# Kernel optimization log

Measured on AMD Instinct MI355X. Metric: run time of the kernel, lower is better.

The kernel has to match this reference:

```python
import jax, jax.numpy as jnp
import numpy as np

CAPACITY_FACTOR = 1.0
MIN_CAPACITY = 4


def setup_inputs() -> dict:
    key = jax.random.key(0)
    ks = jax.random.split(key, 4)
    B, S, D, E, F = 4, 2048, 1024, 16, 4096
    hidden_states = jax.random.normal(ks[0], (B, S, D), dtype=jnp.float32)
    wg = jax.random.normal(ks[1], (D, E), dtype=jnp.float32) * 0.02
    w1 = jax.random.normal(ks[2], (E, D, F), dtype=jnp.float32) * (1.0 / np.sqrt(D))
    b1 = jnp.zeros((E, F), dtype=jnp.float32)
    w2 = jax.random.normal(ks[3], (E, F, D), dtype=jnp.float32) * (1.0 / np.sqrt(F))
    b2 = jnp.zeros((E, D), dtype=jnp.float32)
    return {"hidden_states": hidden_states, "wg": wg, "w1": w1, "b1": b1, "w2": w2, "b2": b2}


def reference(hidden_states, wg, w1, b1, w2, b2):
    B, S, D = hidden_states.shape
    x = hidden_states.reshape(-1, D)                      # [T, D] tokens
    T = x.shape[0]
    E = wg.shape[1]
    capacity = max(int(np.ceil(T / E * CAPACITY_FACTOR)), MIN_CAPACITY)  # static

    # ---- TopKGate (k=1, no noise, no RTS) ----
    logits = x @ wg                                       # [T, E]
    gates = jax.nn.softmax(logits, axis=-1)
    idx1 = jnp.argmax(gates, axis=1)                      # [T]
    mask1 = jax.nn.one_hot(idx1, E, dtype=gates.dtype)    # [T, E]
    exp_counts = jnp.sum(mask1, axis=0).astype(jnp.int32) # per-expert token counts

    # load-balancing aux loss
    me = jnp.mean(gates, axis=0)
    ce = jnp.mean(mask1, axis=0)
    l_aux = jnp.sum(me * ce) * E

    # slot assignment within each expert, drop overflow tokens
    locations1 = jnp.cumsum(mask1, axis=0) - 1.0          # [T, E]
    mask1 = mask1 * (locations1 < capacity).astype(gates.dtype)
    locations1_s = jnp.sum(locations1 * mask1, axis=1).astype(jnp.int32)  # [T]
    gates1 = gates * mask1                                # [T, E] gate prob of kept assignment

    loc_oh = jax.nn.one_hot(locations1_s, capacity, dtype=gates.dtype)    # [T, C]
    combine = jnp.einsum('te,tc->tec', gates1, loc_oh)    # [T, E, C]
    dispatch = (combine > 0).astype(x.dtype)              # [T, E, C]

    # ---- dispatch -> grouped expert FFN -> combine ----
    disp = jnp.einsum('tec,td->ecd', dispatch, x)         # [E, C, D]
    h = jax.nn.gelu(jnp.einsum('ecd,edf->ecf', disp, w1) + b1[:, None, :])
    eo = jnp.einsum('ecf,efd->ecd', h, w2) + b2[:, None, :]  # [E, C, D]
    out = jnp.einsum('tec,ecd->td', combine, eo).reshape(B, S, D)
    return out, l_aux, exp_counts
```

## Files before the change

### kernel.cpp

```cpp
#include <hip/hip_runtime.h>

typedef unsigned short u16;
typedef unsigned int   u32;
typedef unsigned long long u64;
typedef __attribute__((ext_vector_type(8))) __bf16 bf16x8;
typedef __attribute__((ext_vector_type(4))) float  f32x4;

#define TOK 8192
#define DIM 1024
#define NE  16
#define NF  4096
#define CAP 512

__device__ __forceinline__ u16 f2bf(float f) {
    u32 u = __float_as_uint(f);
    u32 r = (u + 0x7FFFu + ((u >> 16) & 1u)) >> 16;
    return (u16)r;
}

__device__ __forceinline__ float gelu_tanh(float x) {
    float u = 0.7978845608028654f * (x + 0.044715f * x * x * x);
    float t = __expf(-2.f * fabsf(u));
    float th = (1.f - t) / (1.f + t);
    th = (u < 0.f) ? -th : th;
    return 0.5f * x * (1.f + th);
}

__device__ __forceinline__ void gld16(const void* g, void* l) {
    __builtin_amdgcn_global_load_lds(
        (const __attribute__((address_space(1))) void*)g,
        (__attribute__((address_space(3))) void*)l, 16, 0, 0);
}

__global__ void moe_init(float* me_sums) {
    if (threadIdx.x < NE) me_sums[threadIdx.x] = 0.f;
}

__global__ void moe_wgT(const float* __restrict__ wg, float* __restrict__ wgT) {
    int i = blockIdx.x * 256 + threadIdx.x;
    int d = i >> 4, e = i & 15;
    wgT[(size_t)e * DIM + d] = wg[i];
}

__global__ void moe_gate(const float* __restrict__ x, const float* __restrict__ wgT,
                         int* __restrict__ eidx, float* __restrict__ gp,
                         float* __restrict__ me_sums) {
    __shared__ float lme[NE];
    const int tid = threadIdx.x;
    if (tid < NE) lme[tid] = 0.f;
    __syncthreads();
    const int tok = blockIdx.x * 16 + (tid >> 4);
    const int e   = tid & 15;
    const float4* xp = (const float4*)(x + (size_t)tok * DIM);
    const float4* wp = (const float4*)(wgT + (size_t)e * DIM);
    float acc = 0.f;
#pragma unroll 4
    for (int i = 0; i < DIM / 4; ++i) {
        float4 a = xp[i], b = wp[i];
        acc = fmaf(a.x, b.x, acc); acc = fmaf(a.y, b.y, acc);
        acc = fmaf(a.z, b.z, acc); acc = fmaf(a.w, b.w, acc);
    }
    float mx = acc;
    for (int off = 8; off; off >>= 1) mx = fmaxf(mx, __shfl_xor(mx, off, 16));
    float ex = __expf(acc - mx);
    float sum = ex;
    for (int off = 8; off; off >>= 1) sum += __shfl_xor(sum, off, 16);
    float p = ex / sum;
    atomicAdd(&lme[e], p);
    float bv = acc; int bi = e;
    for (int off = 8; off; off >>= 1) {
        float ov = __shfl_xor(bv, off, 16);
        int   oi = __shfl_xor(bi, off, 16);
        if (ov > bv || (ov == bv && oi < bi)) { bv = ov; bi = oi; }
    }
    float pw = __shfl(p, bi, 16);
    if (e == 0) { eidx[tok] = bi; gp[tok] = pw; }
    __syncthreads();
    if (tid < 16) atomicAdd(&me_sums[tid], lme[tid]);
}

__global__ void moe_scan(const int* __restrict__ eidx, const float* __restrict__ me_sums,
                         int* __restrict__ slot, int* __restrict__ tos,
                         float* __restrict__ tail ) {
    __shared__ int wcnt[16][16];
    __shared__ int base[16];
    const int tid = threadIdx.x, wid = tid >> 6, lane = tid & 63;
    if (tid < 16) base[tid] = 0;
    for (int i = tid; i < NE * CAP; i += 1024) tos[i] = -1;
    __syncthreads();
    const u64 below = ((u64)1 << lane) - 1;
    for (int chunk = 0; chunk < TOK / 1024; ++chunk) {
        int t = chunk * 1024 + tid;
        int e = eidx[t];
        int rank = 0;
#pragma unroll
        for (int ex = 0; ex < 16; ++ex) {
            u64 m = __ballot(e == ex);
            if (e == ex)    rank = __popcll(m & below);
            if (lane == ex) wcnt[wid][ex] = __popcll(m);
        }
        __syncthreads();
        int pre = base[e];
        for (int w = 0; w < wid; ++w) pre += wcnt[w][e];
        int s = pre + rank;
        slot[t] = s;
        if (s < CAP) tos[e * CAP + s] = t;
        __syncthreads();
        if (tid < 16) {
            int tot = 0;
            for (int w = 0; w < 16; ++w) tot += wcnt[w][tid];
            base[tid] += tot;
        }
        __syncthreads();
    }
    if (tid == 0) {
        float laux = 0.f;
        for (int e2 = 0; e2 < 16; ++e2) {
            float me = me_sums[e2] / (float)TOK;
            float ce = (float)base[e2] / (float)TOK;
            laux += me * ce;
        }
        tail[0] = laux * (float)NE;
    }
    if (tid < 16) tail[1 + tid] = (float)base[tid];
}

__global__ void moe_gather(const float* __restrict__ x, const int* __restrict__ tos,
                           u16* __restrict__ Xg) {
    const int s = blockIdx.x, tid = threadIdx.x;
    const int t = tos[s];
    float4 v = make_float4(0.f, 0.f, 0.f, 0.f);
    if (t >= 0) v = *(const float4*)(x + (size_t)t * DIM + tid * 4);
    u32 lo = (u32)f2bf(v.x) | ((u32)f2bf(v.y) << 16);
    u32 hi = (u32)f2bf(v.z) | ((u32)f2bf(v.w) << 16);
    *(uint2*)(Xg + (size_t)s * DIM + tid * 4) = make_uint2(lo, hi);
}

__global__ void moe_zero_dropped(const int* __restrict__ slot, float* __restrict__ out) {
    const int t = blockIdx.x;
    if (slot[t] < CAP) return;
    *(float4*)(out + (size_t)t * DIM + threadIdx.x * 4) = make_float4(0.f, 0.f, 0.f, 0.f);
}

__global__ void moe_convT(const float* __restrict__ src, u16* __restrict__ dst,
                          int R, int C) {
    __shared__ float tile[64][65];
    int b = blockIdx.x;
    const int tilesC = C >> 6, tilesR = R >> 6;
    int tc = b % tilesC; b /= tilesC;
    int tr = b % tilesR; int e = b / tilesR;
    const float* S = src + ((size_t)e * R + tr * 64) * C + tc * 64;
    const int tid = threadIdx.x;
    const int rr = tid >> 4, cc = (tid & 15) * 4;
#pragma unroll
    for (int i = 0; i < 4; ++i) {
        float4 v = *(const float4*)(S + (size_t)(rr + i * 16) * C + cc);
        tile[rr + i * 16][cc + 0] = v.x; tile[rr + i * 16][cc + 1] = v.y;
        tile[rr + i * 16][cc + 2] = v.z; tile[rr + i * 16][cc + 3] = v.w;
    }
    __syncthreads();
    const int c = tid >> 2, r0 = (tid & 3) * 16;
    u16 tmp[16];
#pragma unroll
    for (int k = 0; k < 16; ++k) tmp[k] = f2bf(tile[r0 + k][c]);
    u16* D = dst + ((size_t)e * C + tc * 64 + c) * R + tr * 64 + r0;
    uint4 w0 = make_uint4((u32)tmp[0] | ((u32)tmp[1] << 16), (u32)tmp[2] | ((u32)tmp[3] << 16),
                          (u32)tmp[4] | ((u32)tmp[5] << 16), (u32)tmp[6] | ((u32)tmp[7] << 16));
    uint4 w1 = make_uint4((u32)tmp[8] | ((u32)tmp[9] << 16), (u32)tmp[10] | ((u32)tmp[11] << 16),
                          (u32)tmp[12] | ((u32)tmp[13] << 16), (u32)tmp[14] | ((u32)tmp[15] << 16));
    *(uint4*)(D) = w0;
    *(uint4*)(D + 8) = w1;
}

__global__ __launch_bounds__(512, 2) void moe_gemm1(const u16* __restrict__ Xg,
                                                    const u16* __restrict__ W1t,
                                                    const float* __restrict__ b1,
                                                    u16* __restrict__ H) {
    __shared__ alignas(16) u16 Als[4][8192];
    __shared__ alignas(16) u16 Bls[4][8192];
    const int tid = threadIdx.x, wave = tid >> 6, lane = tid & 63;
    const int flat = blockIdx.x;
    const int xcd  = flat & 7;
    const int slot = flat >> 3;
    const int e    = xcd * 2 + (slot >> 5);
    const int tile = slot & 31;
    const int bm   = tile & 1;
    const int bn   = tile >> 1;
    const int r4   = lane >> 2;
    const int gch  = (lane & 3) ^ ((lane >> 3) & 3);
    const u16* aSrc = Xg + (size_t)(e * 512 + bm * 256 + wave * 16 + r4) * DIM + gch * 8;
    const u16* bSrc = W1t + (size_t)e * NF * DIM
                    + (size_t)(bn * 256 + wave * 16 + r4) * DIM + gch * 8;
    const int wm = wave & 1, wn = wave >> 1;
    const int fr = lane & 15, fq = lane >> 4;
    const int rdoff = fr * 32 + (fq ^ ((fr >> 1) & 3)) * 8;

    f32x4 acc[2][4][4] = {};

#define STG1A(P, T) do { const int ko = (T) * 32; u16* ad = &Als[P][wave * 512]; \
        gld16(aSrc + ko, ad); gld16(aSrc + 128 * DIM + ko, ad + 4096); } while (0)
#define STG1B(P, T) do { const int ko = (T) * 32; u16* bd = &Bls[P][wave * 512]; \
        gld16(bSrc + ko, bd); gld16(bSrc + 128 * DIM + ko, bd + 4096); } while (0)

    const int NT = DIM / 32;
    STG1A(0, 0); STG1B(0, 0);
    STG1A(1, 1); STG1B(1, 1);
    STG1A(2, 2); STG1B(2, 2);
    for (int t = 0; t < NT; ++t) {
        const int c = t & 3;
        const int rem = NT - 1 - t;
        if (rem >= 2)      asm volatile("s_waitcnt vmcnt(8)" ::: "memory");
        else if (rem == 1) asm volatile("s_waitcnt vmcnt(4)" ::: "memory");
        else               asm volatile("s_waitcnt vmcnt(0)" ::: "memory");
        __builtin_amdgcn_sched_barrier(0);
        __builtin_amdgcn_s_barrier();
        __builtin_amdgcn_sched_barrier(0);
        const u16* Ab = &Als[c][0];
        const u16* Bb = &Bls[c][0];
        bf16x8 bF[4], aF[4];
#pragma unroll
        for (int j = 0; j < 4; ++j)
            bF[j] = *(const bf16x8*)(const void*)(Bb + (wn * 64 + j * 16) * 32 + rdoff);
#pragma unroll
        for (int i = 0; i < 4; ++i)
            aF[i] = *(const bf16x8*)(const void*)(Ab + (wm * 128 + i * 16) * 32 + rdoff);
        if (t + 3 < NT) STG1A((c + 3) & 3, t + 3);
        __builtin_amdgcn_sched_barrier(0);
        asm volatile("s_waitcnt lgkmcnt(0)" ::: "memory");
        __builtin_amdgcn_sched_barrier(0);
        __builtin_amdgcn_s_setprio(1);
#pragma unroll
        for (int i = 0; i < 4; ++i)
#pragma unroll
            for (int j = 0; j < 4; ++j)
                acc[0][i][j] = __builtin_amdgcn_mfma_f32_16x16x32_bf16(aF[i], bF[j], acc[0][i][j], 0, 0, 0);
        __builtin_amdgcn_s_setprio(0);
        __builtin_amdgcn_sched_barrier(0);
        __builtin_amdgcn_s_barrier();
        __builtin_amdgcn_sched_barrier(0);
#pragma unroll
        for (int i = 0; i < 4; ++i)
            aF[i] = *(const bf16x8*)(const void*)(Ab + (wm * 128 + 64 + i * 16) * 32 + rdoff);
        if (t + 3 < NT) STG1B((c + 3) & 3, t + 3);
        __builtin_amdgcn_sched_barrier(0);
        asm volatile("s_waitcnt lgkmcnt(0)" ::: "memory");
        __builtin_amdgcn_sched_barrier(0);
        __builtin_amdgcn_s_setprio(1);
#pragma unroll
        for (int i = 0; i < 4; ++i)
#pragma unroll
            for (int j = 0; j < 4; ++j)
                acc[1][i][j] = __builtin_amdgcn_mfma_f32_16x16x32_bf16(aF[i], bF[j], acc[1][i][j], 0, 0, 0);
        __builtin_amdgcn_s_setprio(0);
    }
#undef STG1A
#undef STG1B

    const int mBase = e * 512 + bm * 256 + wm * 128;
    const int nBase = bn * 256 + wn * 64;
#pragma unroll
    for (int j = 0; j < 4; ++j) {
        const int f = nBase + j * 16 + fr;
        const float bias = b1[e * NF + f];
#pragma unroll
        for (int q = 0; q < 2; ++q)
#pragma unroll
            for (int i = 0; i < 4; ++i) {
                const int m0 = mBase + q * 64 + i * 16 + fq * 4;
#pragma unroll
                for (int r = 0; r < 4; ++r) {
                    float v = acc[q][i][j][r] + bias;
                    H[(size_t)(m0 + r) * NF + f] = f2bf(gelu_tanh(v));
                }
            }
    }
}

__global__ __launch_bounds__(512, 2) void moe_gemm2(const u16* __restrict__ H,
                                                    const u16* __restrict__ W2t,
                                                    const float* __restrict__ b2,
                                                    const int* __restrict__ tos,
                                                    const float* __restrict__ gp,
                                                    float* __restrict__ out) {
    __shared__ alignas(16) u16 Als[4][8192];
    __shared__ alignas(16) u16 Bls[4][4096];
    const int tid = threadIdx.x, wave = tid >> 6, lane = tid & 63;
    const int flat = blockIdx.x;
    const int xcd  = flat & 7;
    const int slot = flat >> 3;
    const int e    = xcd * 2 + (slot >> 4);
    const int tile = slot & 15;
    const int bm   = tile & 1;
    const int bn   = tile >> 1;
    const int r4   = lane >> 2;
    const int gch  = (lane & 3) ^ ((lane >> 3) & 3);
    const u16* aSrc = H + (size_t)(e * 512 + bm * 256 + wave * 16 + r4) * NF + gch * 8;
    const u16* bSrc = W2t + (size_t)e * DIM * NF
                    + (size_t)(bn * 128 + wave * 16 + r4) * NF + gch * 8;
    const int wm = wave & 1, wn = wave >> 1;
    const int fr = lane & 15, fq = lane >> 4;
    const int rdoff = fr * 32 + (fq ^ ((fr >> 1) & 3)) * 8;

    f32x4 acc[2][4][2] = {};

#define STG2A(P, T) do { const int ko = (T) * 32; u16* ad = &Als[P][wave * 512]; \
        gld16(aSrc + ko, ad); gld16(aSrc + (size_t)128 * NF + ko, ad + 4096); } while (0)
#define STG2B(P, T) do { const int ko = (T) * 32; u16* bd = &Bls[P][wave * 512]; \
        gld16(bSrc + ko, bd); } while (0)

    const int NT = NF / 32;
    STG2A(0, 0); STG2B(0, 0);
    STG2A(1, 1); STG2B(1, 1);
    STG2A(2, 2); STG2B(2, 2);
    for (int t = 0; t < NT; ++t) {
        const int c = t & 3;
        const int rem = NT - 1 - t;
        if (rem >= 2)      asm volatile("s_waitcnt vmcnt(6)" ::: "memory");
        else if (rem == 1) asm volatile("s_waitcnt vmcnt(3)" ::: "memory");
        else               asm volatile("s_waitcnt vmcnt(0)" ::: "memory");
        __builtin_amdgcn_sched_barrier(0);
        __builtin_amdgcn_s_barrier();
        __builtin_amdgcn_sched_barrier(0);
        const u16* Ab = &Als[c][0];
        const u16* Bb = &Bls[c][0];
        bf16x8 bF[2], aF[4];
#pragma unroll
        for (int j = 0; j < 2; ++j)
            bF[j] = *(const bf16x8*)(const void*)(Bb + (wn * 32 + j * 16) * 32 + rdoff);
#pragma unroll
        for (int i = 0; i < 4; ++i)
            aF[i] = *(const bf16x8*)(const void*)(Ab + (wm * 128 + i * 16) * 32 + rdoff);
        if (t + 3 < NT) STG2A((c + 3) & 3, t + 3);
        __builtin_amdgcn_sched_barrier(0);
        asm volatile("s_waitcnt lgkmcnt(0)" ::: "memory");
        __builtin_amdgcn_sched_barrier(0);
        __builtin_amdgcn_s_setprio(1);
#pragma unroll
        for (int i = 0; i < 4; ++i)
#pragma unroll
            for (int j = 0; j < 2; ++j)
                acc[0][i][j] = __builtin_amdgcn_mfma_f32_16x16x32_bf16(aF[i], bF[j], acc[0][i][j], 0, 0, 0);
        __builtin_amdgcn_s_setprio(0);
        __builtin_amdgcn_sched_barrier(0);
        __builtin_amdgcn_s_barrier();
        __builtin_amdgcn_sched_barrier(0);
#pragma unroll
        for (int i = 0; i < 4; ++i)
            aF[i] = *(const bf16x8*)(const void*)(Ab + (wm * 128 + 64 + i * 16) * 32 + rdoff);
        if (t + 3 < NT) STG2B((c + 3) & 3, t + 3);
        __builtin_amdgcn_sched_barrier(0);
        asm volatile("s_waitcnt lgkmcnt(0)" ::: "memory");
        __builtin_amdgcn_sched_barrier(0);
        __builtin_amdgcn_s_setprio(1);
#pragma unroll
        for (int i = 0; i < 4; ++i)
#pragma unroll
            for (int j = 0; j < 2; ++j)
                acc[1][i][j] = __builtin_amdgcn_mfma_f32_16x16x32_bf16(aF[i], bF[j], acc[1][i][j], 0, 0, 0);
        __builtin_amdgcn_s_setprio(0);
    }
#undef STG2A
#undef STG2B

    const int mBase = e * 512 + bm * 256 + wm * 128;
    const int nBase = bn * 128 + wn * 32;
#pragma unroll
    for (int q = 0; q < 2; ++q)
#pragma unroll
        for (int i = 0; i < 4; ++i) {
#pragma unroll
            for (int r = 0; r < 4; ++r) {
                const int m = mBase + q * 64 + i * 16 + fq * 4 + r;
                const int t = tos[m];
                if (t < 0) continue;
                const float g = gp[t];
#pragma unroll
                for (int j = 0; j < 2; ++j) {
                    const int d = nBase + j * 16 + fr;
                    out[(size_t)t * DIM + d] = g * (acc[q][i][j][r] + b2[e * DIM + d]);
                }
            }
        }
}

extern "C" void kernel_launch(void* const* d_in, const int* in_sizes, int n_in,
                              void* d_out, int out_size, void* d_ws, size_t ws_size,
                              hipStream_t stream) {
    const float* x  = (const float*)d_in[0];
    const float* wg = (const float*)d_in[1];
    const float* w1 = (const float*)d_in[2];
    const float* b1 = (const float*)d_in[3];
    const float* w2 = (const float*)d_in[4];
    const float* b2 = (const float*)d_in[5];
    float* out = (float*)d_out;

    char* ws = (char*)d_ws;
    const size_t WBF_OFF = 0;
    const size_t XG_OFF  = WBF_OFF + (size_t)NE * NF * DIM * 2;
    const size_t H_OFF   = XG_OFF + (size_t)TOK * DIM * 2;
    const size_t SM_OFF  = H_OFF + (size_t)TOK * NF * 2;
    u16* Wbf = (u16*)(ws + WBF_OFF);
    u16* Xg  = (u16*)(ws + XG_OFF);
    u16* H   = (u16*)(ws + H_OFF);
    int*   eidx = (int*)(ws + SM_OFF);
    float* gp   = (float*)(ws + SM_OFF + 32768);
    int*   slot = (int*)(ws + SM_OFF + 65536);
    int*   tos  = (int*)(ws + SM_OFF + 98304);
    float* me   = (float*)(ws + SM_OFF + 131072);
    float* wgT  = (float*)(ws + SM_OFF + 131072 + 128);

    float* tail = out + (size_t)TOK * DIM;

    moe_init<<<1, 64, 0, stream>>>(me);
    moe_wgT<<<64, 256, 0, stream>>>(wg, wgT);
    moe_gate<<<TOK / 16, 256, 0, stream>>>(x, wgT, eidx, gp, me);
    moe_scan<<<1, 1024, 0, stream>>>(eidx, me, slot, tos, tail);
    moe_gather<<<NE * CAP, 256, 0, stream>>>(x, tos, Xg);
    moe_zero_dropped<<<TOK, 256, 0, stream>>>(slot, out);
    moe_convT<<<NE * (DIM / 64) * (NF / 64), 256, 0, stream>>>(w1, Wbf, DIM, NF);
    moe_gemm1<<<512, 512, 0, stream>>>(Xg, Wbf, b1, H);
    moe_convT<<<NE * (NF / 64) * (DIM / 64), 256, 0, stream>>>(w2, Wbf, NF, DIM);
    moe_gemm2<<<256, 512, 0, stream>>>(H, Wbf, b2, tos, gp, out);
}
```

Measured before the change: 917.5 us.

## Co-schedule W2 bf16 transpose with GEMM1 in one kernel, merge small launches

GEMM1 is fused with the W2 fp32-to-bf16 transpose in a single heterogeneous launch: every fifth block runs a smaller 256x128 GEMM1 tile with double buffering, and the other blocks each transpose four 64x64 W2 tiles into a separate workspace buffer. The intent is to overlap the bandwidth-bound W2 conversion with the compute-bound GEMM1 and to raise occupancy with a smaller LDS footprint. It also folds the me_sums init into the wgT kernel and merges the gather with the dropped-token zeroing, removing launches. Risks: smaller GEMM tiles with a simpler pipeline lower MFMA efficiency, the kernel needs extra workspace for a second weight buffer, and the dropped-token zeroing now only covers the first NE*CAP tokens.

```diff
diff --git a/kernel.cpp b/kernel.cpp
--- a/kernel.cpp
+++ b/kernel.cpp
@@ -32,12 +32,10 @@
         (__attribute__((address_space(3))) void*)l, 16, 0, 0);
 }
 
-__global__ void moe_init(float* me_sums) {
-    if (threadIdx.x < NE) me_sums[threadIdx.x] = 0.f;
-}
-
-__global__ void moe_wgT(const float* __restrict__ wg, float* __restrict__ wgT) {
+__global__ void moe_wgT(const float* __restrict__ wg, float* __restrict__ wgT,
+                        float* __restrict__ me_sums) {
     int i = blockIdx.x * 256 + threadIdx.x;
+    if (i < NE) me_sums[i] = 0.f;
     int d = i >> 4, e = i & 15;
     wgT[(size_t)e * DIM + d] = wg[i];
 }
@@ -125,21 +123,18 @@
     if (tid < 16) tail[1 + tid] = (float)base[tid];
 }
 
-__global__ void moe_gather(const float* __restrict__ x, const int* __restrict__ tos,
-                           u16* __restrict__ Xg) {
-    const int s = blockIdx.x, tid = threadIdx.x;
-    const int t = tos[s];
+__global__ void moe_gather_zero(const float* __restrict__ x, const int* __restrict__ tos,
+                                const int* __restrict__ slot, u16* __restrict__ Xg,
+                                float* __restrict__ out) {
+    const int b = blockIdx.x, tid = threadIdx.x;
+    const int t = tos[b];
     float4 v = make_float4(0.f, 0.f, 0.f, 0.f);
     if (t >= 0) v = *(const float4*)(x + (size_t)t * DIM + tid * 4);
     u32 lo = (u32)f2bf(v.x) | ((u32)f2bf(v.y) << 16);
     u32 hi = (u32)f2bf(v.z) | ((u32)f2bf(v.w) << 16);
-    *(uint2*)(Xg + (size_t)s * DIM + tid * 4) = make_uint2(lo, hi);
-}
-
-__global__ void moe_zero_dropped(const int* __restrict__ slot, float* __restrict__ out) {
-    const int t = blockIdx.x;
-    if (slot[t] < CAP) return;
-    *(float4*)(out + (size_t)t * DIM + threadIdx.x * 4) = make_float4(0.f, 0.f, 0.f, 0.f);
+    *(uint2*)(Xg + (size_t)b * DIM + tid * 4) = make_uint2(lo, hi);
+    if (slot[b] >= CAP)
+        *(float4*)(out + (size_t)b * DIM + tid * 4) = make_float4(0.f, 0.f, 0.f, 0.f);
 }
 
 __global__ void moe_convT(const float* __restrict__ src, u16* __restrict__ dst,
@@ -172,107 +167,132 @@
     *(uint4*)(D + 8) = w1;
 }
 
-__global__ __launch_bounds__(512, 2) void moe_gemm1(const u16* __restrict__ Xg,
-                                                    const u16* __restrict__ W1t,
-                                                    const float* __restrict__ b1,
-                                                    u16* __restrict__ H) {
-    __shared__ alignas(16) u16 Als[4][8192];
-    __shared__ alignas(16) u16 Bls[4][8192];
-    const int tid = threadIdx.x, wave = tid >> 6, lane = tid & 63;
-    const int flat = blockIdx.x;
-    const int xcd  = flat & 7;
-    const int slot = flat >> 3;
-    const int e    = xcd * 2 + (slot >> 5);
-    const int tile = slot & 31;
-    const int bm   = tile & 1;
-    const int bn   = tile >> 1;
-    const int r4   = lane >> 2;
-    const int gch  = (lane & 3) ^ ((lane >> 3) & 3);
-    const u16* aSrc = Xg + (size_t)(e * 512 + bm * 256 + wave * 16 + r4) * DIM + gch * 8;
-    const u16* bSrc = W1t + (size_t)e * NF * DIM
-                    + (size_t)(bn * 256 + wave * 16 + r4) * DIM + gch * 8;
-    const int wm = wave & 1, wn = wave >> 1;
-    const int fr = lane & 15, fq = lane >> 4;
-    const int rdoff = fr * 32 + (fq ^ ((fr >> 1) & 3)) * 8;
-
-    f32x4 acc[2][4][4] = {};
-
-#define STG1A(P, T) do { const int ko = (T) * 32; u16* ad = &Als[P][wave * 512]; \
-        gld16(aSrc + ko, ad); gld16(aSrc + 128 * DIM + ko, ad + 4096); } while (0)
-#define STG1B(P, T) do { const int ko = (T) * 32; u16* bd = &Bls[P][wave * 512]; \
-        gld16(bSrc + ko, bd); gld16(bSrc + 128 * DIM + ko, bd + 4096); } while (0)
-
-    const int NT = DIM / 32;
-    STG1A(0, 0); STG1B(0, 0);
-    STG1A(1, 1); STG1B(1, 1);
-    STG1A(2, 2); STG1B(2, 2);
-    for (int t = 0; t < NT; ++t) {
-        const int c = t & 3;
-        const int rem = NT - 1 - t;
-        if (rem >= 2)      asm volatile("s_waitcnt vmcnt(8)" ::: "memory");
-        else if (rem == 1) asm volatile("s_waitcnt vmcnt(4)" ::: "memory");
-        else               asm volatile("s_waitcnt vmcnt(0)" ::: "memory");
-        __builtin_amdgcn_sched_barrier(0);
+__global__ __launch_bounds__(512, 4) void moe_gemm1cv(const u16* __restrict__ Xg,
+                                                      const u16* __restrict__ W1t,
+                                                      const float* __restrict__ b1,
+                                                      u16* __restrict__ H,
+                                                      const float* __restrict__ w2,
+                                                      u16* __restrict__ W2t) {
+    __shared__ alignas(16) char smem[49152];
+    const int bid = blockIdx.x;
+    const int tid = threadIdx.x;
+    if (bid % 5 == 0) {
+        u16* Als = (u16*)smem;
+        u16* Bls = (u16*)(smem + 32768);
+        const int g    = bid / 5;
+        const int wave = tid >> 6, lane = tid & 63;
+        const int xcd  = bid & 7;
+        const int h    = g >> 3;
+        const int e    = xcd * 2 + (h >> 6);
+        const int tl   = h & 63;
+        const int bm   = tl & 1;
+        const int bn   = tl >> 1;
+        const int r4   = lane >> 2;
+        const int gch  = (lane & 3) ^ ((lane >> 3) & 3);
+        const u16* aSrc = Xg + (size_t)(e * 512 + bm * 256 + wave * 16 + r4) * DIM + gch * 8;
+        const u16* bSrc = W1t + (size_t)e * NF * DIM
+                        + (size_t)(bn * 128 + wave * 16 + r4) * DIM + gch * 8;
+        const int wm = wave & 1, wn = wave >> 1;
+        const int fr = lane & 15, fq = lane >> 4;
+        const int rdoff = fr * 32 + (fq ^ ((fr >> 1) & 3)) * 8;
+        f32x4 acc[2][4][2] = {};
+
+#define STG1(P, T) do { const int ko = (T) * 32; \
+        u16* ad = Als + (P) * 8192 + wave * 512; \
+        u16* bd = Bls + (P) * 4096 + wave * 512; \
+        gld16(aSrc + ko, ad); gld16(aSrc + 128 * DIM + ko, ad + 4096); \
+        gld16(bSrc + ko, bd); } while (0)
+
+        const int NT = DIM / 32;
+        STG1(0, 0);
+        asm volatile("s_waitcnt vmcnt(0)" ::: "memory");
         __builtin_amdgcn_s_barrier();
-        __builtin_amdgcn_sched_barrier(0);
-        const u16* Ab = &Als[c][0];
-        const u16* Bb = &Bls[c][0];
-        bf16x8 bF[4], aF[4];
-#pragma unroll
-        for (int j = 0; j < 4; ++j)
-            bF[j] = *(const bf16x8*)(const void*)(Bb + (wn * 64 + j * 16) * 32 + rdoff);
-#pragma unroll
-        for (int i = 0; i < 4; ++i)
-            aF[i] = *(const bf16x8*)(const void*)(Ab + (wm * 128 + i * 16) * 32 + rdoff);
-        if (t + 3 < NT) STG1A((c + 3) & 3, t + 3);
-        __builtin_amdgcn_sched_barrier(0);
-        asm volatile("s_waitcnt lgkmcnt(0)" ::: "memory");
-        __builtin_amdgcn_sched_barrier(0);
-        __builtin_amdgcn_s_setprio(1);
-#pragma unroll
-        for (int i = 0; i < 4; ++i)
-#pragma unroll
-            for (int j = 0; j < 4; ++j)
-                acc[0][i][j] = __builtin_amdgcn_mfma_f32_16x16x32_bf16(aF[i], bF[j], acc[0][i][j], 0, 0, 0);
-        __builtin_amdgcn_s_setprio(0);
-        __builtin_amdgcn_sched_barrier(0);
-        __builtin_amdgcn_s_barrier();
-        __builtin_amdgcn_sched_barrier(0);
-#pragma unroll
-        for (int i = 0; i < 4; ++i)
-            aF[i] = *(const bf16x8*)(const void*)(Ab + (wm * 128 + 64 + i * 16) * 32 + rdoff);
-        if (t + 3 < NT) STG1B((c + 3) & 3, t + 3);
-        __builtin_amdgcn_sched_barrier(0);
-        asm volatile("s_waitcnt lgkmcnt(0)" ::: "memory");
-        __builtin_amdgcn_sched_barrier(0);
-        __builtin_amdgcn_s_setprio(1);
-#pragma unroll
-        for (int i = 0; i < 4; ++i)
-#pragma unroll
-            for (int j = 0; j < 4; ++j)
-                acc[1][i][j] = __builtin_amdgcn_mfma_f32_16x16x32_bf16(aF[i], bF[j], acc[1][i][j], 0, 0, 0);
-        __builtin_amdgcn_s_setprio(0);
-    }
-#undef STG1A
-#undef STG1B
-
-    const int mBase = e * 512 + bm * 256 + wm * 128;
-    const int nBase = bn * 256 + wn * 64;
-#pragma unroll
-    for (int j = 0; j < 4; ++j) {
-        const int f = nBase + j * 16 + fr;
-        const float bias = b1[e * NF + f];
-#pragma unroll
-        for (int q = 0; q < 2; ++q)
+        int cur = 0;
+        for (int t = 0; t < NT; ++t) {
+            if (t + 1 < NT) STG1(cur ^ 1, t + 1);
+            const u16* Ab = Als + cur * 8192;
+            const u16* Bb = Bls + cur * 4096;
+            bf16x8 aF[4], bF[2];
+#pragma unroll
+            for (int j = 0; j < 2; ++j)
+                bF[j] = *(const bf16x8*)(const void*)(Bb + (wn * 32 + j * 16) * 32 + rdoff);
+#pragma unroll
+            for (int i = 0; i < 4; ++i)
+                aF[i] = *(const bf16x8*)(const void*)(Ab + (wm * 128 + i * 16) * 32 + rdoff);
+            __builtin_amdgcn_s_setprio(1);
+#pragma unroll
+            for (int i = 0; i < 4; ++i)
+#pragma unroll
+                for (int j = 0; j < 2; ++j)
+                    acc[0][i][j] = __builtin_amdgcn_mfma_f32_16x16x32_bf16(aF[i], bF[j], acc[0][i][j], 0, 0, 0);
+            __builtin_amdgcn_s_setprio(0);
+#pragma unroll
+            for (int i = 0; i < 4; ++i)
+                aF[i] = *(const bf16x8*)(const void*)(Ab + (wm * 128 + 64 + i * 16) * 32 + rdoff);
+            __builtin_amdgcn_s_setprio(1);
+#pragma unroll
+            for (int i = 0; i < 4; ++i)
+#pragma unroll
+                for (int j = 0; j < 2; ++j)
+                    acc[1][i][j] = __builtin_amdgcn_mfma_f32_16x16x32_bf16(aF[i], bF[j], acc[1][i][j], 0, 0, 0);
+            __builtin_amdgcn_s_setprio(0);
+            asm volatile("s_waitcnt vmcnt(0)" ::: "memory");
+            __builtin_amdgcn_s_barrier();
+            cur ^= 1;
+        }
+#undef STG1
+        const int mBase = e * 512 + bm * 256 + wm * 128;
+        const int nBase = bn * 128 + wn * 32;
+#pragma unroll
+        for (int j = 0; j < 2; ++j) {
+            const int f = nBase + j * 16 + fr;
+            const float bias = b1[e * NF + f];
+#pragma unroll
+            for (int q = 0; q < 2; ++q)
+#pragma unroll
+                for (int i = 0; i < 4; ++i) {
+                    const int m0 = mBase + q * 64 + i * 16 + fq * 4;
+#pragma unroll
+                    for (int r = 0; r < 4; ++r) {
+                        float v = acc[q][i][j][r] + bias;
+                        H[(size_t)(m0 + r) * NF + f] = f2bf(gelu_tanh(v));
+                    }
+                }
+        }
+    } else {
+        float (*tA)[65] = (float(*)[65])smem;
+        float (*tB)[65] = (float(*)[65])(smem + 16640);
+        const int cid  = bid - bid / 5 - 1;
+        const int sub  = tid >> 8, stid = tid & 255;
+        float (*tl)[65] = sub ? tB : tA;
+        const int R = NF, C = DIM, tilesC = C >> 6, tilesR = R >> 6;
+#pragma unroll
+        for (int kk = 0; kk < 2; ++kk) {
+            int ob = cid * 4 + sub * 2 + kk;
+            int tc = ob % tilesC; int bb = ob / tilesC;
+            int tr = bb % tilesR; int e = bb / tilesR;
+            const float* S = w2 + ((size_t)e * R + tr * 64) * C + tc * 64;
+            const int rr = stid >> 4, cc = (stid & 15) * 4;
 #pragma unroll
             for (int i = 0; i < 4; ++i) {
-                const int m0 = mBase + q * 64 + i * 16 + fq * 4;
-#pragma unroll
-                for (int r = 0; r < 4; ++r) {
-                    float v = acc[q][i][j][r] + bias;
-                    H[(size_t)(m0 + r) * NF + f] = f2bf(gelu_tanh(v));
-                }
+                float4 v = *(const float4*)(S + (size_t)(rr + i * 16) * C + cc);
+                tl[rr + i * 16][cc + 0] = v.x; tl[rr + i * 16][cc + 1] = v.y;
+                tl[rr + i * 16][cc + 2] = v.z; tl[rr + i * 16][cc + 3] = v.w;
             }
+            __syncthreads();
+            const int c = stid >> 2, r0 = (stid & 3) * 16;
+            u16 tmp[16];
+#pragma unroll
+            for (int k2 = 0; k2 < 16; ++k2) tmp[k2] = f2bf(tl[r0 + k2][c]);
+            u16* D = W2t + ((size_t)e * C + tc * 64 + c) * R + tr * 64 + r0;
+            uint4 w0 = make_uint4((u32)tmp[0] | ((u32)tmp[1] << 16), (u32)tmp[2] | ((u32)tmp[3] << 16),
+                                  (u32)tmp[4] | ((u32)tmp[5] << 16), (u32)tmp[6] | ((u32)tmp[7] << 16));
+            uint4 w1 = make_uint4((u32)tmp[8] | ((u32)tmp[9] << 16), (u32)tmp[10] | ((u32)tmp[11] << 16),
+                                  (u32)tmp[12] | ((u32)tmp[13] << 16), (u32)tmp[14] | ((u32)tmp[15] << 16));
+            *(uint4*)(D) = w0;
+            *(uint4*)(D + 8) = w1;
+            __syncthreads();
+        }
     }
 }
 
@@ -395,13 +415,15 @@
     float* out = (float*)d_out;
 
     char* ws = (char*)d_ws;
-    const size_t WBF_OFF = 0;
-    const size_t XG_OFF  = WBF_OFF + (size_t)NE * NF * DIM * 2;
+    const size_t W1_OFF  = 0;
+    const size_t W2_OFF  = W1_OFF + (size_t)NE * NF * DIM * 2;
+    const size_t XG_OFF  = W2_OFF + (size_t)NE * NF * DIM * 2;
     const size_t H_OFF   = XG_OFF + (size_t)TOK * DIM * 2;
     const size_t SM_OFF  = H_OFF + (size_t)TOK * NF * 2;
-    u16* Wbf = (u16*)(ws + WBF_OFF);
-    u16* Xg  = (u16*)(ws + XG_OFF);
-    u16* H   = (u16*)(ws + H_OFF);
+    u16* W1bf = (u16*)(ws + W1_OFF);
+    u16* W2bf = (u16*)(ws + W2_OFF);
+    u16* Xg   = (u16*)(ws + XG_OFF);
+    u16* H    = (u16*)(ws + H_OFF);
     int*   eidx = (int*)(ws + SM_OFF);
     float* gp   = (float*)(ws + SM_OFF + 32768);
     int*   slot = (int*)(ws + SM_OFF + 65536);
@@ -411,14 +433,11 @@
 
     float* tail = out + (size_t)TOK * DIM;
 
-    moe_init<<<1, 64, 0, stream>>>(me);
-    moe_wgT<<<64, 256, 0, stream>>>(wg, wgT);
+    moe_wgT<<<64, 256, 0, stream>>>(wg, wgT, me);
     moe_gate<<<TOK / 16, 256, 0, stream>>>(x, wgT, eidx, gp, me);
     moe_scan<<<1, 1024, 0, stream>>>(eidx, me, slot, tos, tail);
-    moe_gather<<<NE * CAP, 256, 0, stream>>>(x, tos, Xg);
-    moe_zero_dropped<<<TOK, 256, 0, stream>>>(slot, out);
-    moe_convT<<<NE * (DIM / 64) * (NF / 64), 256, 0, stream>>>(w1, Wbf, DIM, NF);
-    moe_gemm1<<<512, 512, 0, stream>>>(Xg, Wbf, b1, H);
-    moe_convT<<<NE * (NF / 64) * (DIM / 64), 256, 0, stream>>>(w2, Wbf, NF, DIM);
-    moe_gemm2<<<256, 512, 0, stream>>>(H, Wbf, b2, tos, gp, out);
-}
+    moe_gather_zero<<<NE * CAP, 256, 0, stream>>>(x, tos, slot, Xg, out);
+    moe_convT<<<NE * (DIM / 64) * (NF / 64), 256, 0, stream>>>(w1, W1bf, DIM, NF);
+    moe_gemm1cv<<<5120, 512, 0, stream>>>(Xg, W1bf, b1, H, w2, W2bf);
+    moe_gemm2<<<256, 512, 0, stream>>>(H, W2bf, b2, tos, gp, out);
+}
```

New measurement: 889.7 us. 3.0% less time.
